# Performance work log

Measured on AMD Instinct MI355X. Metric: run time of the kernel, lower is better.

Reference implementation:

```python
import jax, jax.numpy as jnp
import numpy as np

B, N, DIM = 2, 4096, 512
HEADS, DIM_HEAD = 8, 64
INNER = HEADS * DIM_HEAD  # 512
SCALE = DIM_HEAD ** -0.5
LN_EPS = 1e-5


def setup_inputs() -> dict:
    key = jax.random.key(0)
    ks = jax.random.split(key, 4)
    x = jax.random.normal(ks[0], (B, N, DIM), dtype=jnp.float32)
    # weights stored as [in, out] for plain matmul
    w_qkv = jax.random.normal(ks[1], (DIM, 3 * INNER), dtype=jnp.float32) * (DIM ** -0.5)
    ln_gamma = jnp.ones((INNER,), dtype=jnp.float32)
    ln_beta = jnp.zeros((INNER,), dtype=jnp.float32)
    w_out = jax.random.normal(ks[2], (INNER, DIM), dtype=jnp.float32) * (INNER ** -0.5)
    b_out = jnp.zeros((DIM,), dtype=jnp.float32)
    return {"x": x, "w_qkv": w_qkv, "ln_gamma": ln_gamma, "ln_beta": ln_beta,
            "w_out": w_out, "b_out": b_out}


def _layernorm(x, gamma, beta):
    mu = jnp.mean(x, axis=-1, keepdims=True)
    var = jnp.mean(jnp.square(x - mu), axis=-1, keepdims=True)
    return (x - mu) * jax.lax.rsqrt(var + LN_EPS) * gamma + beta


def reference(x, w_qkv, ln_gamma, ln_beta, w_out, b_out):
    b, n, _ = x.shape
    qkv = x @ w_qkv                                   # [b, n, 3*inner]
    q, k, v = jnp.split(qkv, 3, axis=-1)
    def to_heads(t):
        return t.reshape(b, n, HEADS, DIM_HEAD).transpose(0, 2, 1, 3)  # [b,h,n,d]
    q, k, v = to_heads(q), to_heads(k), to_heads(v)
    dots = jnp.einsum('bhid,bhjd->bhij', q, k) * SCALE  # [b,h,n,n]
    attn = jax.nn.relu(dots)                            # non-softmax rectified attention
    out = jnp.einsum('bhij,bhjd->bhid', attn, v)        # [b,h,n,d]
    out = out.transpose(0, 2, 1, 3).reshape(b, n, INNER)
    out = _layernorm(out, ln_gamma, ln_beta)
    return out @ w_out + b_out                          # [b,n,dim]
```

## Files before the change

### kernel.cpp

```cpp
#include <hip/hip_runtime.h>
#include <stdint.h>
#include <stddef.h>

typedef __bf16 bf16;
typedef bf16 bf16x4 __attribute__((ext_vector_type(4)));
typedef bf16 bf16x8 __attribute__((ext_vector_type(8)));
typedef float f32x4 __attribute__((ext_vector_type(4)));

#define DEVI static __device__ __forceinline__


DEVI f32x4 mfma16(bf16x8 a, bf16x8 b, f32x4 c) {
  return __builtin_amdgcn_mfma_f32_16x16x32_bf16(a, b, c, 0, 0, 0);
}

DEVI void gload_lds16(const bf16* g, bf16* lds) {
  __builtin_amdgcn_global_load_lds(
      (const __attribute__((address_space(1))) unsigned int*)g,
      (__attribute__((address_space(3))) unsigned int*)lds, 16, 0, 0);
}


__global__ __launch_bounds__(256) void cvt_kernel(const float* __restrict__ in,
                                                  bf16* __restrict__ out, int n4) {
  int i = blockIdx.x * blockDim.x + threadIdx.x;
  const int stride = gridDim.x * blockDim.x;
  for (; i < n4; i += stride) {
    f32x4 v = reinterpret_cast<const f32x4*>(in)[i];
    bf16x4 o;
    o[0] = (bf16)v[0]; o[1] = (bf16)v[1]; o[2] = (bf16)v[2]; o[3] = (bf16)v[3];
    reinterpret_cast<bf16x4*>(out)[i] = o;
  }
}

__global__ __launch_bounds__(256) void tcvt_kernel(const float* __restrict__ in,
                                                   bf16* __restrict__ out, int Kd, int Nd) {
  int i = blockIdx.x * blockDim.x + threadIdx.x;
  const int total = Kd * Nd;
  const int stride = gridDim.x * blockDim.x;
  for (; i < total; i += stride) {
    int k = i / Nd, n = i - k * Nd;
    out[(size_t)n * Kd + k] = (bf16)in[i];
  }
}

template <int EPI>
__global__ __launch_bounds__(256) void gemm_kernel(
    const bf16* __restrict__ A, const bf16* __restrict__ BT,
    bf16* __restrict__ qo, bf16* __restrict__ ko, bf16* __restrict__ vto,
    const float* __restrict__ bias, float* __restrict__ fo) {
  constexpr int K = 512;
  __shared__ __align__(16) bf16 As[128 * 64];
  __shared__ __align__(16) bf16 Bs[128 * 64];
  const int lane = threadIdx.x & 63;
  const int w = threadIdx.x >> 6;
  const int wm = w >> 1, wn = w & 1;
  const int m0 = blockIdx.y * 128, n0 = blockIdx.x * 128;
  const int sl = lane >> 3;
  const int ssc = ((lane & 7) ^ sl) * 8;

  f32x4 acc[4][4];
#pragma unroll
  for (int i = 0; i < 4; ++i)
#pragma unroll
    for (int j = 0; j < 4; ++j) acc[i][j] = {0.f, 0.f, 0.f, 0.f};

  for (int kt = 0; kt < K / 64; ++kt) {
    const int k0 = kt * 64;
    __syncthreads();
#pragma unroll
    for (int c = 0; c < 4; ++c) {
      const int ca = w * 4 + c;
      const int trow = ca * 8 + sl;
      gload_lds16(A + (size_t)(m0 + trow) * K + k0 + ssc, As + ca * 512);
      gload_lds16(BT + (size_t)(n0 + trow) * K + k0 + ssc, Bs + ca * 512);
    }
    __syncthreads();
#pragma unroll
    for (int kc = 0; kc < 2; ++kc) {
      const int cs = kc * 4 + (lane >> 4);
      const int csw = (cs ^ (lane & 7)) * 8;
      bf16x8 af[4], bfr[4];
#pragma unroll
      for (int mi = 0; mi < 4; ++mi)
        af[mi] = *reinterpret_cast<const bf16x8*>(
            &As[(wm * 64 + mi * 16 + (lane & 15)) * 64 + csw]);
#pragma unroll
      for (int ni = 0; ni < 4; ++ni)
        bfr[ni] = *reinterpret_cast<const bf16x8*>(
            &Bs[(wn * 64 + ni * 16 + (lane & 15)) * 64 + csw]);
#pragma unroll
      for (int mi = 0; mi < 4; ++mi)
#pragma unroll
        for (int ni = 0; ni < 4; ++ni)
          acc[mi][ni] = mfma16(af[mi], bfr[ni], acc[mi][ni]);
    }
  }

#pragma unroll
  for (int mi = 0; mi < 4; ++mi) {
#pragma unroll
    for (int ni = 0; ni < 4; ++ni) {
#pragma unroll
      for (int r = 0; r < 4; ++r) {
        const int m = m0 + wm * 64 + mi * 16 + (lane >> 4) * 4 + r;
        const int col = n0 + wn * 64 + ni * 16 + (lane & 15);
        const float v = acc[mi][ni][r];
        if (EPI == 0) {
          const int b = m >> 12, n = m & 4095;
          const int sec = col >> 9, jj = col & 511, h = jj >> 6, d = jj & 63;
          const int bh = b * 8 + h;
          const bf16 hv = (bf16)v;
          if (sec == 0)
            qo[((size_t)bh * 4096 + n) * 64 + d] = hv;
          else if (sec == 1)
            ko[((size_t)bh * 4096 + n) * 64 + d] = hv;
          else
            vto[((size_t)bh * 64 + d) * 4096 + n] = hv;
        } else {
          fo[(size_t)m * 512 + col] = v + bias[col];
        }
      }
    }
  }
}

__global__ __launch_bounds__(256) void attn_kernel(
    const bf16* __restrict__ Q, const bf16* __restrict__ Kg,
    const bf16* __restrict__ VT, float* __restrict__ out0,
    float* __restrict__ out1) {
  __shared__ __align__(16) bf16 Ks[2 * 64 * 64];
  __shared__ __align__(16) bf16 Vs[2 * 64 * 64];
  __shared__ __align__(16) bf16 Ps[4][32 * 64];
  const int lane = threadIdx.x & 63;
  const int w = threadIdx.x >> 6;
  const int hi = lane >> 4;
  const int bh = blockIdx.y;
  const int q0 = blockIdx.x * 128 + w * 32;
  const int kvbase = blockIdx.z * 2048;
  const bf16* Qh = Q + (size_t)bh * 4096 * 64;
  const bf16* Kh = Kg + (size_t)bh * 4096 * 64;
  const bf16* Vh = VT + (size_t)bh * 64 * 4096;
  float* outp = blockIdx.z ? out1 : out0;

  const int sl = lane >> 3;
  const int ssc = ((lane & 7) ^ sl) * 8;

  auto stage = [&](int bi, int kv0) {
    bf16* KsB = Ks + bi * 4096;
    bf16* VsB = Vs + bi * 4096;
    if (w < 2) {
#pragma unroll
      for (int c = 0; c < 4; ++c) {
        const int ca = w * 4 + c;
        const int r = ca * 8 + sl;
        gload_lds16(Kh + (size_t)(kv0 + r) * 64 + ssc, KsB + ca * 512);
      }
    } else {
#pragma unroll
      for (int c = 0; c < 4; ++c) {
        const int ca = (w - 2) * 4 + c;
        const int d = ca * 8 + sl;
        gload_lds16(Vh + (size_t)d * 4096 + kv0 + ssc, VsB + ca * 512);
      }
    }
  };

  bf16x8 qf[2][2];
#pragma unroll
  for (int qb = 0; qb < 2; ++qb)
#pragma unroll
    for (int kc = 0; kc < 2; ++kc)
      qf[qb][kc] = *reinterpret_cast<const bf16x8*>(
          &Qh[(size_t)(q0 + qb * 16 + (lane & 15)) * 64 + kc * 32 + hi * 8]);

  f32x4 o[2][4];
#pragma unroll
  for (int qb = 0; qb < 2; ++qb)
#pragma unroll
    for (int db = 0; db < 4; ++db) o[qb][db] = {0.f, 0.f, 0.f, 0.f};

  bf16* Pw = Ps[w];

  stage(0, kvbase);
  asm volatile("s_waitcnt vmcnt(0)" ::: "memory");
  __builtin_amdgcn_s_barrier();

  for (int it = 0; it < 32; ++it) {
    const int kv0 = kvbase + it * 64;
    const int cur = it & 1;
    const bf16* KsC = Ks + cur * 4096;
    const bf16* VsC = Vs + cur * 4096;
    if (it < 31) stage(cur ^ 1, kv0 + 64);

    f32x4 s[2][4];
#pragma unroll
    for (int qb = 0; qb < 2; ++qb)
#pragma unroll
      for (int kvb = 0; kvb < 4; ++kvb) s[qb][kvb] = {0.f, 0.f, 0.f, 0.f};
#pragma unroll
    for (int kc = 0; kc < 2; ++kc) {
      const int csw = ((kc * 4 + hi) ^ (lane & 7)) * 8;
      bf16x8 kf[4];
#pragma unroll
      for (int kvb = 0; kvb < 4; ++kvb)
        kf[kvb] = *reinterpret_cast<const bf16x8*>(
            &KsC[(kvb * 16 + (lane & 15)) * 64 + csw]);
      __builtin_amdgcn_s_setprio(1);
#pragma unroll
      for (int qb = 0; qb < 2; ++qb)
#pragma unroll
        for (int kvb = 0; kvb < 4; ++kvb)
          s[qb][kvb] = mfma16(kf[kvb], qf[qb][kc], s[qb][kvb]);
      __builtin_amdgcn_s_setprio(0);
    }

#pragma unroll
    for (int qb = 0; qb < 2; ++qb) {
      const int prow = qb * 16 + (lane & 15);
      const int swz = (prow & 7) << 3;
#pragma unroll
      for (int kvb = 0; kvb < 4; ++kvb) {
        bf16x4 pq;
#pragma unroll
        for (int r = 0; r < 4; ++r) {
          float v = s[qb][kvb][r];
          pq[r] = (bf16)(v > 0.f ? v : 0.f);
        }
        const int ebase = (kvb * 16 + hi * 4) ^ swz;
        *reinterpret_cast<bf16x4*>(&Pw[prow * 64 + ebase]) = pq;
      }
    }

#pragma unroll
    for (int kc = 0; kc < 2; ++kc) {
      const int csw = ((kc * 4 + hi) ^ (lane & 7)) * 8;
      bf16x8 pf[2], vf[4];
#pragma unroll
      for (int qb = 0; qb < 2; ++qb)
        pf[qb] = *reinterpret_cast<const bf16x8*>(
            &Pw[(qb * 16 + (lane & 15)) * 64 + csw]);
#pragma unroll
      for (int db = 0; db < 4; ++db)
        vf[db] = *reinterpret_cast<const bf16x8*>(
            &VsC[(db * 16 + (lane & 15)) * 64 + csw]);
      __builtin_amdgcn_s_setprio(1);
#pragma unroll
      for (int qb = 0; qb < 2; ++qb)
#pragma unroll
        for (int db = 0; db < 4; ++db)
          o[qb][db] = mfma16(pf[qb], vf[db], o[qb][db]);
      __builtin_amdgcn_s_setprio(0);
    }

    asm volatile("s_waitcnt vmcnt(0)" ::: "memory");
    __builtin_amdgcn_s_barrier();
  }

  const int b = bh >> 3, h = bh & 7;
#pragma unroll
  for (int qb = 0; qb < 2; ++qb)
#pragma unroll
    for (int db = 0; db < 4; ++db)
#pragma unroll
      for (int r = 0; r < 4; ++r) {
        const int n = q0 + qb * 16 + hi * 4 + r;
        const int dcol = db * 16 + (lane & 15);
        outp[((size_t)(b * 4096 + n)) * 512 + h * 64 + dcol] = o[qb][db][r] * 0.125f;
      }
}

__global__ __launch_bounds__(256) void ln_kernel(const float* __restrict__ in0,
                                                 const float* __restrict__ in1,
                                                 const float* __restrict__ gamma,
                                                 const float* __restrict__ beta,
                                                 bf16* __restrict__ out) {
  const int lane = threadIdx.x & 63;
  const int w = threadIdx.x >> 6;
  const int row = blockIdx.x * 4 + w;
  const float* r0 = in0 + (size_t)row * 512;
  const float* r1 = in1 + (size_t)row * 512;
  f32x4 a = *reinterpret_cast<const f32x4*>(&r0[lane * 4]);
  f32x4 b = *reinterpret_cast<const f32x4*>(&r0[256 + lane * 4]);
  f32x4 a1 = *reinterpret_cast<const f32x4*>(&r1[lane * 4]);
  f32x4 b1 = *reinterpret_cast<const f32x4*>(&r1[256 + lane * 4]);
#pragma unroll
  for (int i = 0; i < 4; ++i) { a[i] += a1[i]; b[i] += b1[i]; }
  float s = a[0] + a[1] + a[2] + a[3] + b[0] + b[1] + b[2] + b[3];
  float ss = a[0] * a[0] + a[1] * a[1] + a[2] * a[2] + a[3] * a[3] +
             b[0] * b[0] + b[1] * b[1] + b[2] * b[2] + b[3] * b[3];
#pragma unroll
  for (int off = 32; off > 0; off >>= 1) {
    s += __shfl_xor(s, off);
    ss += __shfl_xor(ss, off);
  }
  const float mean = s * (1.f / 512.f);
  const float var = ss * (1.f / 512.f) - mean * mean;
  const float rstd = rsqrtf(var + 1e-5f);
  f32x4 g0 = *reinterpret_cast<const f32x4*>(&gamma[lane * 4]);
  f32x4 g1 = *reinterpret_cast<const f32x4*>(&gamma[256 + lane * 4]);
  f32x4 e0 = *reinterpret_cast<const f32x4*>(&beta[lane * 4]);
  f32x4 e1 = *reinterpret_cast<const f32x4*>(&beta[256 + lane * 4]);
  bf16x4 o0, o1;
#pragma unroll
  for (int i = 0; i < 4; ++i) {
    o0[i] = (bf16)((a[i] - mean) * rstd * g0[i] + e0[i]);
    o1[i] = (bf16)((b[i] - mean) * rstd * g1[i] + e1[i]);
  }
  *reinterpret_cast<bf16x4*>(&out[(size_t)row * 512 + lane * 4]) = o0;
  *reinterpret_cast<bf16x4*>(&out[(size_t)row * 512 + 256 + lane * 4]) = o1;
}

extern "C" void kernel_launch(void* const* d_in, const int* in_sizes, int n_in,
                              void* d_out, int out_size, void* d_ws, size_t ws_size,
                              hipStream_t stream) {
  const float* x = (const float*)d_in[0];
  const float* w_qkv = (const float*)d_in[1];
  const float* ln_g = (const float*)d_in[2];
  const float* ln_b = (const float*)d_in[3];
  const float* w_out = (const float*)d_in[4];
  const float* b_out = (const float*)d_in[5];
  float* out = (float*)d_out;

  char* ws = (char*)d_ws;
  size_t off = 0;
  auto alloc = [&](size_t bytes) {
    void* p = ws + off;
    off += (bytes + 255) & ~(size_t)255;
    return p;
  };
  bf16* x_bf = (bf16*)alloc((size_t)8192 * 512 * 2);
  bf16* wqkvT = (bf16*)alloc((size_t)1536 * 512 * 2);
  bf16* woutT = (bf16*)alloc((size_t)512 * 512 * 2);
  bf16* qbuf = (bf16*)alloc((size_t)16 * 4096 * 64 * 2);
  bf16* kbuf = (bf16*)alloc((size_t)16 * 4096 * 64 * 2);
  bf16* vtbuf = (bf16*)alloc((size_t)16 * 64 * 4096 * 2);
  float* attn_out0 = (float*)alloc((size_t)8192 * 512 * 4);
  float* attn_out1 = (float*)alloc((size_t)8192 * 512 * 4);
  bf16* ln_bf = (bf16*)alloc((size_t)8192 * 512 * 2);

  cvt_kernel<<<2048, 256, 0, stream>>>(x, x_bf, 8192 * 512 / 4);
  tcvt_kernel<<<1024, 256, 0, stream>>>(w_qkv, wqkvT, 512, 1536);
  tcvt_kernel<<<512, 256, 0, stream>>>(w_out, woutT, 512, 512);

  gemm_kernel<0><<<dim3(12, 64), 256, 0, stream>>>(x_bf, wqkvT, qbuf, kbuf, vtbuf,
                                                   nullptr, nullptr);

  attn_kernel<<<dim3(32, 16, 2), 256, 0, stream>>>(qbuf, kbuf, vtbuf,
                                                   attn_out0, attn_out1);

  ln_kernel<<<2048, 256, 0, stream>>>(attn_out0, attn_out1, ln_g, ln_b, ln_bf);

  gemm_kernel<1><<<dim3(4, 64), 256, 0, stream>>>(ln_bf, woutT, nullptr, nullptr,
                                                  nullptr, b_out, out);
}
```

Baseline: 224.2 us.

## Keep ReLU probabilities in registers and double per-wave query tile in attention

The attention kernel drops the LDS round trip for the ReLU'd score tile. It permutes the K rows it stages (sigma64) so that the S accumulator layout lines up directly with the A-operand layout of the P·V MFMA, and P is packed in registers. Each wave now handles 64 queries instead of 32, halving the grid and raising K/V reuse at the cost of more accumulator registers (launch bounds set to 2). Separately, the QKV GEMM epilogue transposes the V section through LDS so V^T is written with coalesced 16-byte stores instead of scattered 2-byte stores.

```diff
diff --git a/kernel.cpp b/kernel.cpp
--- a/kernel.cpp
+++ b/kernel.cpp
@@ -19,6 +19,8 @@
       (const __attribute__((address_space(1))) unsigned int*)g,
       (__attribute__((address_space(3))) unsigned int*)lds, 16, 0, 0);
 }
+
+DEVI int sigma64(int r) { return (r & 0x23) | ((r & 0xC) << 1) | ((r & 0x10) >> 2); }
 
 
 __global__ __launch_bounds__(256) void cvt_kernel(const float* __restrict__ in,
@@ -50,10 +52,12 @@
     bf16* __restrict__ qo, bf16* __restrict__ ko, bf16* __restrict__ vto,
     const float* __restrict__ bias, float* __restrict__ fo) {
   constexpr int K = 512;
-  __shared__ __align__(16) bf16 As[128 * 64];
-  __shared__ __align__(16) bf16 Bs[128 * 64];
+  __shared__ __align__(16) bf16 SMEM[128 * 136];
+  bf16* As = SMEM;
+  bf16* Bs = SMEM + 128 * 64;
   const int lane = threadIdx.x & 63;
   const int w = threadIdx.x >> 6;
+  const int hi = lane >> 4;
   const int wm = w >> 1, wn = w & 1;
   const int m0 = blockIdx.y * 128, n0 = blockIdx.x * 128;
   const int sl = lane >> 3;
@@ -78,7 +82,7 @@
     __syncthreads();
 #pragma unroll
     for (int kc = 0; kc < 2; ++kc) {
-      const int cs = kc * 4 + (lane >> 4);
+      const int cs = kc * 4 + hi;
       const int csw = (cs ^ (lane & 7)) * 8;
       bf16x8 af[4], bfr[4];
 #pragma unroll
@@ -97,13 +101,39 @@
     }
   }
 
+  if (EPI == 0 && n0 >= 1024) {
+    __syncthreads();
+#pragma unroll
+    for (int mi = 0; mi < 4; ++mi)
+#pragma unroll
+      for (int ni = 0; ni < 4; ++ni)
+#pragma unroll
+        for (int r = 0; r < 4; ++r) {
+          const int rl = wm * 64 + mi * 16 + hi * 4 + r;
+          const int cl = wn * 64 + ni * 16 + (lane & 15);
+          SMEM[cl * 136 + rl] = (bf16)acc[mi][ni][r];
+        }
+    __syncthreads();
+    const int b = m0 >> 12, nb = m0 & 4095;
+    const int jj0 = n0 - 1024;
+    const int cl = threadIdx.x >> 1, half = threadIdx.x & 1;
+    const int jj = jj0 + cl, h = jj >> 6, d = jj & 63;
+    bf16* dst = vto + ((size_t)(b * 8 + h) * 64 + d) * 4096 + nb + half * 64;
+    const bf16* src = SMEM + cl * 136 + half * 64;
+#pragma unroll
+    for (int j = 0; j < 8; ++j)
+      *reinterpret_cast<bf16x8*>(dst + j * 8) =
+          *reinterpret_cast<const bf16x8*>(src + j * 8);
+    return;
+  }
+
 #pragma unroll
   for (int mi = 0; mi < 4; ++mi) {
 #pragma unroll
     for (int ni = 0; ni < 4; ++ni) {
 #pragma unroll
       for (int r = 0; r < 4; ++r) {
-        const int m = m0 + wm * 64 + mi * 16 + (lane >> 4) * 4 + r;
+        const int m = m0 + wm * 64 + mi * 16 + hi * 4 + r;
         const int col = n0 + wn * 64 + ni * 16 + (lane & 15);
         const float v = acc[mi][ni][r];
         if (EPI == 0) {
@@ -113,10 +143,8 @@
           const bf16 hv = (bf16)v;
           if (sec == 0)
             qo[((size_t)bh * 4096 + n) * 64 + d] = hv;
-          else if (sec == 1)
+          else
             ko[((size_t)bh * 4096 + n) * 64 + d] = hv;
-          else
-            vto[((size_t)bh * 64 + d) * 4096 + n] = hv;
         } else {
           fo[(size_t)m * 512 + col] = v + bias[col];
         }
@@ -125,18 +153,18 @@
   }
 }
 
-__global__ __launch_bounds__(256) void attn_kernel(
+__global__ __launch_bounds__(256, 2) void attn_kernel(
     const bf16* __restrict__ Q, const bf16* __restrict__ Kg,
     const bf16* __restrict__ VT, float* __restrict__ out0,
     float* __restrict__ out1) {
   __shared__ __align__(16) bf16 Ks[2 * 64 * 64];
   __shared__ __align__(16) bf16 Vs[2 * 64 * 64];
-  __shared__ __align__(16) bf16 Ps[4][32 * 64];
   const int lane = threadIdx.x & 63;
   const int w = threadIdx.x >> 6;
   const int hi = lane >> 4;
+  const int ql = lane & 15;
   const int bh = blockIdx.y;
-  const int q0 = blockIdx.x * 128 + w * 32;
+  const int q0 = blockIdx.x * 256 + w * 64;
   const int kvbase = blockIdx.z * 2048;
   const bf16* Qh = Q + (size_t)bh * 4096 * 64;
   const bf16* Kh = Kg + (size_t)bh * 4096 * 64;
@@ -146,41 +174,48 @@
   const int sl = lane >> 3;
   const int ssc = ((lane & 7) ^ sl) * 8;
 
+  int soff[4];
+  if (w < 2) {
+#pragma unroll
+    for (int c = 0; c < 4; ++c) {
+      const int rho = (w * 4 + c) * 8 + sl;
+      soff[c] = sigma64(rho) * 64 + ssc;
+    }
+  } else {
+#pragma unroll
+    for (int c = 0; c < 4; ++c) {
+      const int d = ((w - 2) * 4 + c) * 8 + sl;
+      soff[c] = d * 4096 + ssc;
+    }
+  }
+
   auto stage = [&](int bi, int kv0) {
-    bf16* KsB = Ks + bi * 4096;
-    bf16* VsB = Vs + bi * 4096;
     if (w < 2) {
-#pragma unroll
-      for (int c = 0; c < 4; ++c) {
-        const int ca = w * 4 + c;
-        const int r = ca * 8 + sl;
-        gload_lds16(Kh + (size_t)(kv0 + r) * 64 + ssc, KsB + ca * 512);
-      }
+      bf16* KsB = Ks + bi * 4096;
+#pragma unroll
+      for (int c = 0; c < 4; ++c)
+        gload_lds16(Kh + (size_t)kv0 * 64 + soff[c], KsB + (w * 4 + c) * 512);
     } else {
-#pragma unroll
-      for (int c = 0; c < 4; ++c) {
-        const int ca = (w - 2) * 4 + c;
-        const int d = ca * 8 + sl;
-        gload_lds16(Vh + (size_t)d * 4096 + kv0 + ssc, VsB + ca * 512);
-      }
+      bf16* VsB = Vs + bi * 4096;
+#pragma unroll
+      for (int c = 0; c < 4; ++c)
+        gload_lds16(Vh + kv0 + soff[c], VsB + ((w - 2) * 4 + c) * 512);
     }
   };
 
-  bf16x8 qf[2][2];
-#pragma unroll
-  for (int qb = 0; qb < 2; ++qb)
+  bf16x8 qf[4][2];
+#pragma unroll
+  for (int qb = 0; qb < 4; ++qb)
 #pragma unroll
     for (int kc = 0; kc < 2; ++kc)
       qf[qb][kc] = *reinterpret_cast<const bf16x8*>(
-          &Qh[(size_t)(q0 + qb * 16 + (lane & 15)) * 64 + kc * 32 + hi * 8]);
-
-  f32x4 o[2][4];
-#pragma unroll
-  for (int qb = 0; qb < 2; ++qb)
+          &Qh[(size_t)(q0 + qb * 16 + ql) * 64 + kc * 32 + hi * 8]);
+
+  f32x4 o[4][4];
+#pragma unroll
+  for (int qb = 0; qb < 4; ++qb)
 #pragma unroll
     for (int db = 0; db < 4; ++db) o[qb][db] = {0.f, 0.f, 0.f, 0.f};
-
-  bf16* Pw = Ps[w];
 
   stage(0, kvbase);
   asm volatile("s_waitcnt vmcnt(0)" ::: "memory");
@@ -193,9 +228,9 @@
     const bf16* VsC = Vs + cur * 4096;
     if (it < 31) stage(cur ^ 1, kv0 + 64);
 
-    f32x4 s[2][4];
-#pragma unroll
-    for (int qb = 0; qb < 2; ++qb)
+    f32x4 s[4][4];
+#pragma unroll
+    for (int qb = 0; qb < 4; ++qb)
 #pragma unroll
       for (int kvb = 0; kvb < 4; ++kvb) s[qb][kvb] = {0.f, 0.f, 0.f, 0.f};
 #pragma unroll
@@ -205,10 +240,10 @@
 #pragma unroll
       for (int kvb = 0; kvb < 4; ++kvb)
         kf[kvb] = *reinterpret_cast<const bf16x8*>(
-            &KsC[(kvb * 16 + (lane & 15)) * 64 + csw]);
+            &KsC[(kvb * 16 + ql) * 64 + csw]);
       __builtin_amdgcn_s_setprio(1);
 #pragma unroll
-      for (int qb = 0; qb < 2; ++qb)
+      for (int qb = 0; qb < 4; ++qb)
 #pragma unroll
         for (int kvb = 0; kvb < 4; ++kvb)
           s[qb][kvb] = mfma16(kf[kvb], qf[qb][kc], s[qb][kvb]);
@@ -216,40 +251,27 @@
     }
 
 #pragma unroll
-    for (int qb = 0; qb < 2; ++qb) {
-      const int prow = qb * 16 + (lane & 15);
-      const int swz = (prow & 7) << 3;
-#pragma unroll
-      for (int kvb = 0; kvb < 4; ++kvb) {
-        bf16x4 pq;
-#pragma unroll
-        for (int r = 0; r < 4; ++r) {
-          float v = s[qb][kvb][r];
-          pq[r] = (bf16)(v > 0.f ? v : 0.f);
-        }
-        const int ebase = (kvb * 16 + hi * 4) ^ swz;
-        *reinterpret_cast<bf16x4*>(&Pw[prow * 64 + ebase]) = pq;
-      }
-    }
-
-#pragma unroll
     for (int kc = 0; kc < 2; ++kc) {
       const int csw = ((kc * 4 + hi) ^ (lane & 7)) * 8;
-      bf16x8 pf[2], vf[4];
-#pragma unroll
-      for (int qb = 0; qb < 2; ++qb)
-        pf[qb] = *reinterpret_cast<const bf16x8*>(
-            &Pw[(qb * 16 + (lane & 15)) * 64 + csw]);
+      bf16x8 vf[4];
 #pragma unroll
       for (int db = 0; db < 4; ++db)
         vf[db] = *reinterpret_cast<const bf16x8*>(
-            &VsC[(db * 16 + (lane & 15)) * 64 + csw]);
+            &VsC[(db * 16 + ql) * 64 + csw]);
+      bf16x8 pa[4];
+#pragma unroll
+      for (int qb = 0; qb < 4; ++qb)
+#pragma unroll
+        for (int u = 0; u < 2; ++u)
+#pragma unroll
+          for (int r = 0; r < 4; ++r)
+            pa[qb][u * 4 + r] = (bf16)fmaxf(s[qb][2 * kc + u][r], 0.f);
       __builtin_amdgcn_s_setprio(1);
 #pragma unroll
-      for (int qb = 0; qb < 2; ++qb)
+      for (int qb = 0; qb < 4; ++qb)
 #pragma unroll
         for (int db = 0; db < 4; ++db)
-          o[qb][db] = mfma16(pf[qb], vf[db], o[qb][db]);
+          o[qb][db] = mfma16(pa[qb], vf[db], o[qb][db]);
       __builtin_amdgcn_s_setprio(0);
     }
 
@@ -259,13 +281,13 @@
 
   const int b = bh >> 3, h = bh & 7;
 #pragma unroll
-  for (int qb = 0; qb < 2; ++qb)
+  for (int qb = 0; qb < 4; ++qb)
 #pragma unroll
     for (int db = 0; db < 4; ++db)
 #pragma unroll
       for (int r = 0; r < 4; ++r) {
         const int n = q0 + qb * 16 + hi * 4 + r;
-        const int dcol = db * 16 + (lane & 15);
+        const int dcol = db * 16 + ql;
         outp[((size_t)(b * 4096 + n)) * 512 + h * 64 + dcol] = o[qb][db][r] * 0.125f;
       }
 }
@@ -346,7 +368,7 @@
   gemm_kernel<0><<<dim3(12, 64), 256, 0, stream>>>(x_bf, wqkvT, qbuf, kbuf, vtbuf,
                                                    nullptr, nullptr);
 
-  attn_kernel<<<dim3(32, 16, 2), 256, 0, stream>>>(qbuf, kbuf, vtbuf,
+  attn_kernel<<<dim3(16, 16, 2), 256, 0, stream>>>(qbuf, kbuf, vtbuf,
                                                    attn_out0, attn_out1);
 
   ln_kernel<<<2048, 256, 0, stream>>>(attn_out0, attn_out1, ln_g, ln_b, ln_bf);
```

After: 191.6 us. -14.5%, faster.
